# Performance work log

Measured on AMD Instinct MI355X. Metric: run time of the kernel, lower is better.

## Reference

```python
import jax, jax.numpy as jnp
import numpy as np

D_MODEL = 768
NUM_HEADS = 12
D_K = D_MODEL // NUM_HEADS


def setup_inputs() -> dict:
    key = jax.random.key(0)
    ks = jax.random.split(key, 9)
    B, S = 2, 4096
    x = jax.random.normal(ks[0], (B, S, D_MODEL), dtype=jnp.float32)
    s = 1.0 / np.sqrt(D_MODEL)
    Wq = jax.random.normal(ks[1], (D_MODEL, D_MODEL), dtype=jnp.float32) * s
    Wk = jax.random.normal(ks[2], (D_MODEL, D_MODEL), dtype=jnp.float32) * s
    Wv = jax.random.normal(ks[3], (D_MODEL, D_MODEL), dtype=jnp.float32) * s
    Wo = jax.random.normal(ks[4], (D_MODEL, D_MODEL), dtype=jnp.float32) * s
    bq = jnp.zeros((D_MODEL,), dtype=jnp.float32)
    bk = jnp.zeros((D_MODEL,), dtype=jnp.float32)
    bv = jnp.zeros((D_MODEL,), dtype=jnp.float32)
    bo = jnp.zeros((D_MODEL,), dtype=jnp.float32)
    return {"x": x, "Wq": Wq, "bq": bq, "Wk": Wk, "bk": bk,
            "Wv": Wv, "bv": bv, "Wo": Wo, "bo": bo}


def _split_heads(t):
    B, S, _ = t.shape
    return t.reshape(B, S, NUM_HEADS, D_K).transpose(0, 2, 1, 3)  # [B,H,S,d_k]


def reference(x, Wq, bq, Wk, bk, Wv, bv, Wo, bo):
    Q = _split_heads(x @ Wq.T + bq)
    K = _split_heads(x @ Wk.T + bk)
    V = _split_heads(x @ Wv.T + bv)
    scale = 1.0 / jnp.sqrt(jnp.float32(D_K))
    scores = jnp.einsum('bhqd,bhkd->bhqk', Q, K) * scale  # [B,H,S,S]
    attn = jax.nn.softmax(scores, axis=-1)
    out = jnp.einsum('bhqk,bhkd->bhqd', attn, V)          # [B,H,S,d_k]
    B, _, S, _ = out.shape
    out = out.transpose(0, 2, 1, 3).reshape(B, S, D_MODEL)
    return out @ Wo.T + bo
```

## Files before the change

kernel.cpp:

```cpp
#include <hip/hip_runtime.h>
#include <hip/hip_bf16.h>
#include <stdint.h>

typedef __hip_bfloat16 bf16;
typedef __attribute__((ext_vector_type(8))) short short8;
typedef __attribute__((ext_vector_type(4))) float f32x4;
typedef __attribute__((ext_vector_type(16))) float f32x16;

#define MFMA16(a, b, c) __builtin_amdgcn_mfma_f32_16x16x32_bf16((a), (b), (c), 0, 0, 0)
#define MFMA32(a, b, c) __builtin_amdgcn_mfma_f32_32x32x16_bf16((a), (b), (c), 0, 0, 0)

__device__ __forceinline__ unsigned short f2bf(float f) {
  bf16 h = __float2bfloat16(f);
  unsigned short u;
  __builtin_memcpy(&u, &h, 2);
  return u;
}

__device__ __forceinline__ uint32_t cvtpk(float lo, float hi) {
  uint32_t r;
  asm("v_cvt_pk_bf16_f32 %0, %1, %2" : "=v"(r) : "v"(lo), "v"(hi));
  return r;
}

__device__ __forceinline__ void pl32swap(uint32_t& a, uint32_t& b) {
  asm volatile("v_permlane32_swap_b32 %0, %1" : "+v"(a), "+v"(b));
}

__device__ __forceinline__ void gload_lds16(const void* g, void* l) {
  __builtin_amdgcn_global_load_lds(
      (const __attribute__((address_space(1))) uint32_t*)g,
      (__attribute__((address_space(3))) uint32_t*)l, 16, 0, 0);
}

__device__ __forceinline__ int swz_chunk(int row, int c) { return c ^ (row & 7); }

__global__ __launch_bounds__(256) void cvt_all(
    const float* __restrict__ x,
    const float* __restrict__ w0, const float* __restrict__ w1,
    const float* __restrict__ w2, const float* __restrict__ w3,
    bf16* __restrict__ xo,
    bf16* __restrict__ o0, bf16* __restrict__ o1,
    bf16* __restrict__ o2, bf16* __restrict__ o3) {
  int idx = blockIdx.x * 256 + threadIdx.x;
  const float* src;
  bf16* dst;
  int i;
  if (idx < 1572864) {
    src = x; dst = xo; i = idx;
  } else {
    int r = idx - 1572864;
    int w = r / 147456;
    i = r - w * 147456;
    src = (w == 0) ? w0 : (w == 1) ? w1 : (w == 2) ? w2 : w3;
    dst = (w == 0) ? o0 : (w == 1) ? o1 : (w == 2) ? o2 : o3;
  }
  float4 v = ((const float4*)src)[i];
  ushort4 u;
  u.x = f2bf(v.x); u.y = f2bf(v.y); u.z = f2bf(v.z); u.w = f2bf(v.w);
  ((ushort4*)dst)[i] = u;
}

__global__ __launch_bounds__(256, 4) void gemm_qkv(
    const bf16* __restrict__ A,
    const bf16* __restrict__ Wqb, const bf16* __restrict__ Wkb,
    const bf16* __restrict__ Wvb,
    const float* __restrict__ bq, const float* __restrict__ bk,
    const float* __restrict__ bv,
    bf16* __restrict__ Qh, bf16* __restrict__ Kh, bf16* __restrict__ Vtt,
    float sq) {
  __shared__ bf16 As[128 * 64];
  __shared__ bf16 Bs[128 * 64];
  const int tid = threadIdx.x;
  const int lane = tid & 63, wid = tid >> 6;
  const int wr = wid >> 1, wc = wid & 1;
  const int l15 = lane & 15, lhi = lane >> 4;
  const int tm = blockIdx.x * 128;
  const int by = blockIdx.y;
  const int seg = by / 6;
  const int tn = (by - seg * 6) * 128;

  const bf16* B = (seg == 0) ? Wqb : (seg == 1) ? Wkb : Wvb;
  const float* bias = (seg == 0) ? bq : (seg == 1) ? bk : bv;
  const float scale = (seg == 0) ? sq : 1.0f;
  const int K = 768;

  f32x4 zero = {0.f, 0.f, 0.f, 0.f};
  f32x4 acc[4][4];
  for (int i = 0; i < 4; ++i)
    for (int j = 0; j < 4; ++j) acc[i][j] = zero;

  for (int k0 = 0; k0 < K; k0 += 64) {
    __syncthreads();
    for (int it = 0; it < 4; ++it) {
      int o = (tid + it * 256) << 4;
      int row = o >> 7, c = (o >> 4) & 7;
      int sw = swz_chunk(row, c) << 4;
      gload_lds16((const char*)A + (((size_t)(tm + row) * K + k0) << 1) + sw, (char*)As + o);
      gload_lds16((const char*)B + (((size_t)(tn + row) * K + k0) << 1) + sw, (char*)Bs + o);
    }
    __syncthreads();
    for (int ks = 0; ks < 2; ++ks) {
      short8 af[4], bfr[4];
      for (int mi = 0; mi < 4; ++mi) {
        int row = wr * 64 + mi * 16 + l15;
        af[mi] = *(const short8*)((const char*)As + row * 128 +
                                  (swz_chunk(row, ks * 4 + lhi) << 4));
      }
      for (int ni = 0; ni < 4; ++ni) {
        int row = wc * 64 + ni * 16 + l15;
        bfr[ni] = *(const short8*)((const char*)Bs + row * 128 +
                                   (swz_chunk(row, ks * 4 + lhi) << 4));
      }
      for (int mi = 0; mi < 4; ++mi)
        for (int ni = 0; ni < 4; ++ni)
          acc[mi][ni] = MFMA16(af[mi], bfr[ni], acc[mi][ni]);
    }
  }

  if (seg == 2) {
    for (int mi = 0; mi < 4; ++mi)
      for (int ni = 0; ni < 4; ++ni) {
        int m0 = tm + wr * 64 + mi * 16 + lhi * 4;
        int n = tn + wc * 64 + ni * 16 + l15;
        int b = m0 >> 12, s = m0 & 4095, hh = n >> 6, d = n & 63;
        float bia = bias[n];
        ushort4 us;
        us.x = f2bf(acc[mi][ni][0] + bia);
        us.y = f2bf(acc[mi][ni][1] + bia);
        us.z = f2bf(acc[mi][ni][2] + bia);
        us.w = f2bf(acc[mi][ni][3] + bia);
        size_t e = (size_t)(b * 12 + hh) * 262144 + (size_t)(s >> 6) * 4096 +
                   (size_t)((s >> 3) & 7) * 512 + d * 8 + (s & 7);
        *(ushort4*)(Vtt + e) = us;
      }
  } else {
    bf16* dst = (seg == 0) ? Qh : Kh;
    for (int mi = 0; mi < 4; ++mi)
      for (int ni = 0; ni < 4; ++ni)
        for (int j = 0; j < 4; ++j) {
          int m = tm + wr * 64 + mi * 16 + lhi * 4 + j;
          int n = tn + wc * 64 + ni * 16 + l15;
          float v = (acc[mi][ni][j] + bias[n]) * scale;
          int b = m >> 12, s = m & 4095, hh = n >> 6, d = n & 63;
          dst[(((size_t)(b * 12 + hh) * 4096 + s) << 6) + d] = __float2bfloat16(v);
        }
  }
}

__global__ __launch_bounds__(256, 4) void gemm_wo(
    const bf16* __restrict__ A, const bf16* __restrict__ B,
    const float* __restrict__ bias, float* __restrict__ C) {
  __shared__ bf16 As[128 * 64];
  __shared__ bf16 Bs[64 * 64];
  const int tid = threadIdx.x;
  const int lane = tid & 63, wid = tid >> 6;
  const int l15 = lane & 15, lhi = lane >> 4;
  const int tm = blockIdx.x * 128, tn = blockIdx.y * 64;
  const int K = 768;

  f32x4 zero = {0.f, 0.f, 0.f, 0.f};
  f32x4 acc[2][4];
  for (int i = 0; i < 2; ++i)
    for (int j = 0; j < 4; ++j) acc[i][j] = zero;

  for (int k0 = 0; k0 < K; k0 += 64) {
    __syncthreads();
    for (int it = 0; it < 4; ++it) {
      int o = (tid + it * 256) << 4;
      int row = o >> 7, c = (o >> 4) & 7;
      int sw = swz_chunk(row, c) << 4;
      gload_lds16((const char*)A + (((size_t)(tm + row) * K + k0) << 1) + sw, (char*)As + o);
    }
    for (int it = 0; it < 2; ++it) {
      int o = (tid + it * 256) << 4;
      int row = o >> 7, c = (o >> 4) & 7;
      int sw = swz_chunk(row, c) << 4;
      gload_lds16((const char*)B + (((size_t)(tn + row) * K + k0) << 1) + sw, (char*)Bs + o);
    }
    __syncthreads();
    for (int ks = 0; ks < 2; ++ks) {
      short8 af[2], bfr[4];
      for (int mi = 0; mi < 2; ++mi) {
        int row = wid * 32 + mi * 16 + l15;
        af[mi] = *(const short8*)((const char*)As + row * 128 +
                                  (swz_chunk(row, ks * 4 + lhi) << 4));
      }
      for (int ni = 0; ni < 4; ++ni) {
        int row = ni * 16 + l15;
        bfr[ni] = *(const short8*)((const char*)Bs + row * 128 +
                                   (swz_chunk(row, ks * 4 + lhi) << 4));
      }
      for (int mi = 0; mi < 2; ++mi)
        for (int ni = 0; ni < 4; ++ni)
          acc[mi][ni] = MFMA16(af[mi], bfr[ni], acc[mi][ni]);
    }
  }

  for (int mi = 0; mi < 2; ++mi)
    for (int ni = 0; ni < 4; ++ni)
      for (int j = 0; j < 4; ++j) {
        int m = tm + wid * 32 + mi * 16 + lhi * 4 + j;
        int n = tn + ni * 16 + l15;
        C[(size_t)m * 768 + n] = acc[mi][ni][j] + bias[n];
      }
}

__global__ __launch_bounds__(256, 3) void attn_kernel(
    const bf16* __restrict__ Qh, const bf16* __restrict__ Kh,
    const bf16* __restrict__ VTT, bf16* __restrict__ AO) {
  __shared__ float4 smem4[34816 / 16];
  char* smraw = (char*)smem4;
#define KT(b) (smraw + (b) * 8192)
#define VT(b) (smraw + 16384 + (b) * 8192)
  float* OX = (float*)smraw;

  const int tid = threadIdx.x;
  const int lane = tid & 63, wid = tid >> 6;
  const int l31 = lane & 31, h = lane >> 5;
  const int qsub = wid & 1, kvh = wid >> 1;

  const int i = blockIdx.x;
  const int xcd = i & 7, slot = i >> 3;
  const int bh = xcd * 3 + (slot >> 5);
  const int qt = slot & 31;

  const size_t hb = (size_t)bh * 262144;
  const bf16* Qb = Qh + hb;
  const bf16* Kb = Kh + hb;
  const char* Vbc = (const char*)(VTT + hb);
  const int qb = qt * 128 + qsub * 64;

  short8 qf[2][4];
#pragma unroll
  for (int j = 0; j < 2; ++j)
#pragma unroll
    for (int ki = 0; ki < 4; ++ki)
      qf[j][ki] = *(const short8*)((const char*)Qb + (size_t)(qb + 32 * j + l31) * 128 +
                                   ki * 32 + h * 16);

  f32x16 z16;
  for (int i2 = 0; i2 < 16; ++i2) z16[i2] = 0.f;
  f32x16 o00 = z16, o01 = z16, o10 = z16, o11 = z16;
  float psum0 = 0.f, psum1 = 0.f;

  const int krow = kvh * 32 + l31;

  for (int it = 0; it < 2; ++it) {
    int o = (tid + it * 256) << 4;
    int row = o >> 7, c = (o >> 4) & 7;
    gload_lds16((const char*)Kb + row * 128 + (swz_chunk(row, c) << 4), KT(0) + o);
    gload_lds16(Vbc + (swz_chunk(row, c) << 10) + (row << 4), VT(0) + o);
  }
  __syncthreads();

  int cur = 0;
  for (int kt = 0; kt < 64; ++kt) {
    if (kt < 63) {
      const char* Kg = (const char*)(Kb + (size_t)(kt + 1) * 4096);
      const char* Vg = Vbc + (size_t)(kt + 1) * 8192;
      char* Kd = KT(cur ^ 1);
      char* Vd = VT(cur ^ 1);
      for (int it = 0; it < 2; ++it) {
        int o = (tid + it * 256) << 4;
        int row = o >> 7, c = (o >> 4) & 7;
        gload_lds16(Kg + row * 128 + (swz_chunk(row, c) << 4), Kd + o);
        gload_lds16(Vg + (swz_chunk(row, c) << 10) + (row << 4), Vd + o);
      }
    }

    const char* Kl = KT(cur);
    const char* Vl = VT(cur);

    f32x16 s0, s1;
    __builtin_amdgcn_s_setprio(1);
    {
      short8 kf = *(const short8*)(Kl + krow * 128 + (swz_chunk(krow, h) << 4));
      s0 = MFMA32(kf, qf[0][0], z16);
      s1 = MFMA32(kf, qf[1][0], z16);
    }
#pragma unroll
    for (int ki = 1; ki < 4; ++ki) {
      short8 kf = *(const short8*)(Kl + krow * 128 + (swz_chunk(krow, 2 * ki + h) << 4));
      s0 = MFMA32(kf, qf[0][ki], s0);
      s1 = MFMA32(kf, qf[1][ki], s1);
    }
    __builtin_amdgcn_s_setprio(0);

    short8 pb[2][2];
#pragma unroll
    for (int j = 0; j < 2; ++j) {
#pragma unroll
      for (int kk = 0; kk < 2; ++kk) {
        float p[8];
#pragma unroll
        for (int e = 0; e < 8; ++e)
          p[e] = __builtin_amdgcn_exp2f(j ? s1[8 * kk + e] : s0[8 * kk + e]);
        float ps = ((p[0] + p[1]) + (p[2] + p[3])) + ((p[4] + p[5]) + (p[6] + p[7]));
        if (j) psum1 += ps; else psum0 += ps;
        uint32_t A0 = cvtpk(p[0], p[1]), A1 = cvtpk(p[2], p[3]);
        uint32_t B0 = cvtpk(p[4], p[5]), B1 = cvtpk(p[6], p[7]);
        pl32swap(A0, B0);
        pl32swap(A1, B1);
        uint32_t w[4] = {A0, A1, B0, B1};
        short8 frag;
        __builtin_memcpy(&frag, w, 16);
        pb[j][kk] = frag;
      }
    }

    __builtin_amdgcn_s_setprio(1);
#pragma unroll
    for (int kk = 0; kk < 2; ++kk) {
      short8 v0 = *(const short8*)(Vl + l31 * 128 +
                                   (swz_chunk(l31, 4 * kvh + 2 * kk + h) << 4));
      short8 v1 = *(const short8*)(Vl + (32 + l31) * 128 +
                                   (swz_chunk(32 + l31, 4 * kvh + 2 * kk + h) << 4));
      o00 = MFMA32(v0, pb[0][kk], o00);
      o01 = MFMA32(v0, pb[1][kk], o01);
      o10 = MFMA32(v1, pb[0][kk], o10);
      o11 = MFMA32(v1, pb[1][kk], o11);
    }
    __builtin_amdgcn_s_setprio(0);

    __syncthreads();
    cur ^= 1;
  }

  psum0 += __shfl_xor(psum0, 32);
  psum1 += __shfl_xor(psum1, 32);

  float* W = OX + (size_t)(qsub * 64 + lane) * 68;
  if (kvh == 1) {
#pragma unroll
    for (int g = 0; g < 4; ++g) {
      *(float4*)(W + 0 * 16 + 4 * g) = make_float4(o00[4*g], o00[4*g+1], o00[4*g+2], o00[4*g+3]);
      *(float4*)(W + 1 * 16 + 4 * g) = make_float4(o01[4*g], o01[4*g+1], o01[4*g+2], o01[4*g+3]);
      *(float4*)(W + 2 * 16 + 4 * g) = make_float4(o10[4*g], o10[4*g+1], o10[4*g+2], o10[4*g+3]);
      *(float4*)(W + 3 * 16 + 4 * g) = make_float4(o11[4*g], o11[4*g+1], o11[4*g+2], o11[4*g+3]);
    }
    W[64] = psum0;
    W[65] = psum1;
  }
  __syncthreads();
  if (kvh == 0) {
#pragma unroll
    for (int g = 0; g < 4; ++g) {
      float4 a0 = *(const float4*)(W + 0 * 16 + 4 * g);
      float4 a1 = *(const float4*)(W + 1 * 16 + 4 * g);
      float4 a2 = *(const float4*)(W + 2 * 16 + 4 * g);
      float4 a3 = *(const float4*)(W + 3 * 16 + 4 * g);
      o00[4*g] += a0.x; o00[4*g+1] += a0.y; o00[4*g+2] += a0.z; o00[4*g+3] += a0.w;
      o01[4*g] += a1.x; o01[4*g+1] += a1.y; o01[4*g+2] += a1.z; o01[4*g+3] += a1.w;
      o10[4*g] += a2.x; o10[4*g+1] += a2.y; o10[4*g+2] += a2.z; o10[4*g+3] += a2.w;
      o11[4*g] += a3.x; o11[4*g+1] += a3.y; o11[4*g+2] += a3.z; o11[4*g+3] += a3.w;
    }
    psum0 += W[64];
    psum1 += W[65];
    float pinv0 = 1.0f / psum0;
    float pinv1 = 1.0f / psum1;

    const int b = bh / 12, hd = bh % 12;
#pragma unroll
    for (int j = 0; j < 2; ++j) {
      int q = qb + 32 * j + l31;
      char* base = (char*)AO + (((size_t)(b * 4096 + q)) * 768 + hd * 64) * 2;
      float pv = j ? pinv1 : pinv0;
#pragma unroll
      for (int t = 0; t < 2; ++t) {
#pragma unroll
        for (int u = 0; u < 4; ++u) {
          ushort4 us;
          float v0 = (t ? (j ? o11[4*u+0] : o10[4*u+0]) : (j ? o01[4*u+0] : o00[4*u+0]));
          float v1 = (t ? (j ? o11[4*u+1] : o10[4*u+1]) : (j ? o01[4*u+1] : o00[4*u+1]));
          float v2 = (t ? (j ? o11[4*u+2] : o10[4*u+2]) : (j ? o01[4*u+2] : o00[4*u+2]));
          float v3 = (t ? (j ? o11[4*u+3] : o10[4*u+3]) : (j ? o01[4*u+3] : o00[4*u+3]));
          us.x = f2bf(v0 * pv);
          us.y = f2bf(v1 * pv);
          us.z = f2bf(v2 * pv);
          us.w = f2bf(v3 * pv);
          int d0 = 32 * t + 8 * u + 4 * h;
          *(ushort4*)(base + d0 * 2) = us;
        }
      }
    }
  }
#undef KT
#undef VT
}

extern "C" void kernel_launch(void* const* d_in, const int* in_sizes, int n_in,
                              void* d_out, int out_size, void* d_ws, size_t ws_size,
                              hipStream_t stream) {
  (void)in_sizes; (void)n_in; (void)out_size; (void)ws_size;
  const float* x  = (const float*)d_in[0];
  const float* Wq = (const float*)d_in[1];
  const float* bq = (const float*)d_in[2];
  const float* Wk = (const float*)d_in[3];
  const float* bk = (const float*)d_in[4];
  const float* Wv = (const float*)d_in[5];
  const float* bv = (const float*)d_in[6];
  const float* Wo = (const float*)d_in[7];
  const float* bo = (const float*)d_in[8];

  char* ws = (char*)d_ws;
  bf16* Qh  = (bf16*)(ws + 0);
  bf16* Kh  = (bf16*)(ws + 12582912);
  bf16* VTT = (bf16*)(ws + 25165824);
  bf16* xb  = (bf16*)(ws + 37748736);
  bf16* Wqb = (bf16*)(ws + 50331648);
  bf16* Wkb = (bf16*)(ws + 51511296);
  bf16* Wvb = (bf16*)(ws + 52690944);
  bf16* Wob = (bf16*)(ws + 53870592);
  bf16* AO  = xb;

  cvt_all<<<8448, 256, 0, stream>>>(x, Wq, Wk, Wv, Wo, xb, Wqb, Wkb, Wvb, Wob);

  const float SQ = 0.125f * 1.4426950408889634f;
  dim3 gq(64, 18);
  gemm_qkv<<<gq, 256, 0, stream>>>(xb, Wqb, Wkb, Wvb, bq, bk, bv,
                                   Qh, Kh, VTT, SQ);
  attn_kernel<<<768, 256, 0, stream>>>(Qh, Kh, VTT, AO);
  dim3 gw(64, 12);
  gemm_wo<<<gw, 256, 0, stream>>>(AO, Wob, bo, (float*)d_out);
}
```

Baseline: 180.3 us.

## Software-pipeline attention loop so QK of next tile overlaps PV of previous

```diff
diff --git a/kernel.cpp b/kernel.cpp
--- a/kernel.cpp
+++ b/kernel.cpp
@@ -209,10 +209,10 @@
 __global__ __launch_bounds__(256, 3) void attn_kernel(
     const bf16* __restrict__ Qh, const bf16* __restrict__ Kh,
     const bf16* __restrict__ VTT, bf16* __restrict__ AO) {
-  __shared__ float4 smem4[34816 / 16];
+  __shared__ float4 smem4[40960 / 16];
   char* smraw = (char*)smem4;
-#define KT(b) (smraw + (b) * 8192)
-#define VT(b) (smraw + 16384 + (b) * 8192)
+#define KTB(b) (smraw + (b) * 8192)
+#define VTB(b) (smraw + 16384 + (b) * 8192)
   float* OX = (float*)smraw;
 
   const int tid = threadIdx.x;
@@ -246,86 +246,120 @@
 
   const int krow = kvh * 32 + l31;
 
-  for (int it = 0; it < 2; ++it) {
-    int o = (tid + it * 256) << 4;
-    int row = o >> 7, c = (o >> 4) & 7;
-    gload_lds16((const char*)Kb + row * 128 + (swz_chunk(row, c) << 4), KT(0) + o);
-    gload_lds16(Vbc + (swz_chunk(row, c) << 10) + (row << 4), VT(0) + o);
-  }
+#define STAGE_K(kt, dstb)                                                  \
+  for (int it = 0; it < 2; ++it) {                                         \
+    int o = (tid + it * 256) << 4;                                         \
+    int row = o >> 7, c = (o >> 4) & 7;                                    \
+    gload_lds16((const char*)Kb + (size_t)(kt) * 4096 * 2 / 2 * 2 + 0 +    \
+                    (size_t)(kt) * 0 + (size_t)(kt) * 8192 - (size_t)(kt) * 8192 + \
+                    (size_t)(kt) * 8192 + row * 128 + (swz_chunk(row, c) << 4), \
+                (dstb) + o);                                               \
+  }
+#undef STAGE_K
+#define STAGE_K(kt, dstb)                                                  \
+  for (int it = 0; it < 2; ++it) {                                         \
+    int o = (tid + it * 256) << 4;                                         \
+    int row = o >> 7, c = (o >> 4) & 7;                                    \
+    gload_lds16((const char*)Kb + (size_t)(kt) * 8192 + row * 128 +        \
+                    (swz_chunk(row, c) << 4),                              \
+                (dstb) + o);                                               \
+  }
+#define STAGE_V(kt, dstb)                                                  \
+  for (int it = 0; it < 2; ++it) {                                         \
+    int o = (tid + it * 256) << 4;                                         \
+    int row = o >> 7, c = (o >> 4) & 7;                                    \
+    gload_lds16(Vbc + (size_t)(kt) * 8192 + (swz_chunk(row, c) << 10) +    \
+                    (row << 4),                                            \
+                (dstb) + o);                                               \
+  }
+
+#define DO_QK(Kl)                                                          \
+  {                                                                        \
+    short8 kf = *(const short8*)((Kl) + krow * 128 + (swz_chunk(krow, h) << 4)); \
+    s0 = MFMA32(kf, qf[0][0], z16);                                        \
+    s1 = MFMA32(kf, qf[1][0], z16);                                        \
+  }                                                                        \
+  _Pragma("unroll")                                                        \
+  for (int ki = 1; ki < 4; ++ki) {                                         \
+    short8 kf = *(const short8*)((Kl) + krow * 128 +                       \
+                                 (swz_chunk(krow, 2 * ki + h) << 4));      \
+    s0 = MFMA32(kf, qf[0][ki], s0);                                        \
+    s1 = MFMA32(kf, qf[1][ki], s1);                                        \
+  }
+
+#define DO_PV(Vl)                                                          \
+  _Pragma("unroll")                                                        \
+  for (int kk = 0; kk < 2; ++kk) {                                         \
+    short8 v0 = *(const short8*)((Vl) + l31 * 128 +                        \
+                                 (swz_chunk(l31, 4 * kvh + 2 * kk + h) << 4)); \
+    short8 v1 = *(const short8*)((Vl) + (32 + l31) * 128 +                 \
+                                 (swz_chunk(32 + l31, 4 * kvh + 2 * kk + h) << 4)); \
+    o00 = MFMA32(v0, pb[0][kk], o00);                                      \
+    o01 = MFMA32(v0, pb[1][kk], o01);                                      \
+    o10 = MFMA32(v1, pb[0][kk], o10);                                      \
+    o11 = MFMA32(v1, pb[1][kk], o11);                                      \
+  }
+
+#define DO_EXP()                                                           \
+  _Pragma("unroll")                                                        \
+  for (int j = 0; j < 2; ++j) {                                            \
+    _Pragma("unroll")                                                      \
+    for (int kk = 0; kk < 2; ++kk) {                                       \
+      float p[8];                                                          \
+      _Pragma("unroll")                                                    \
+      for (int e = 0; e < 8; ++e)                                          \
+        p[e] = __builtin_amdgcn_exp2f(j ? s1[8 * kk + e] : s0[8 * kk + e]); \
+      float ps = ((p[0] + p[1]) + (p[2] + p[3])) + ((p[4] + p[5]) + (p[6] + p[7])); \
+      if (j) psum1 += ps; else psum0 += ps;                                \
+      uint32_t A0 = cvtpk(p[0], p[1]), A1 = cvtpk(p[2], p[3]);             \
+      uint32_t B0 = cvtpk(p[4], p[5]), B1 = cvtpk(p[6], p[7]);             \
+      pl32swap(A0, B0);                                                    \
+      pl32swap(A1, B1);                                                    \
+      uint32_t w_[4] = {A0, A1, B0, B1};                                   \
+      short8 frag;                                                         \
+      __builtin_memcpy(&frag, w_, 16);                                     \
+      pb[j][kk] = frag;                                                    \
+    }                                                                      \
+  }
+
+  short8 pb[2][2];
+
+  STAGE_K(0, KTB(0));
+  STAGE_V(0, VTB(0));
   __syncthreads();
-
-  int cur = 0;
-  for (int kt = 0; kt < 64; ++kt) {
-    if (kt < 63) {
-      const char* Kg = (const char*)(Kb + (size_t)(kt + 1) * 4096);
-      const char* Vg = Vbc + (size_t)(kt + 1) * 8192;
-      char* Kd = KT(cur ^ 1);
-      char* Vd = VT(cur ^ 1);
-      for (int it = 0; it < 2; ++it) {
-        int o = (tid + it * 256) << 4;
-        int row = o >> 7, c = (o >> 4) & 7;
-        gload_lds16(Kg + row * 128 + (swz_chunk(row, c) << 4), Kd + o);
-        gload_lds16(Vg + (swz_chunk(row, c) << 10) + (row << 4), Vd + o);
-      }
-    }
-
-    const char* Kl = KT(cur);
-    const char* Vl = VT(cur);
-
+  STAGE_K(1, KTB(1));
+  STAGE_V(1, VTB(1));
+  {
     f32x16 s0, s1;
     __builtin_amdgcn_s_setprio(1);
-    {
-      short8 kf = *(const short8*)(Kl + krow * 128 + (swz_chunk(krow, h) << 4));
-      s0 = MFMA32(kf, qf[0][0], z16);
-      s1 = MFMA32(kf, qf[1][0], z16);
-    }
-#pragma unroll
-    for (int ki = 1; ki < 4; ++ki) {
-      short8 kf = *(const short8*)(Kl + krow * 128 + (swz_chunk(krow, 2 * ki + h) << 4));
-      s0 = MFMA32(kf, qf[0][ki], s0);
-      s1 = MFMA32(kf, qf[1][ki], s1);
-    }
+    DO_QK(KTB(0));
     __builtin_amdgcn_s_setprio(0);
-
-    short8 pb[2][2];
-#pragma unroll
-    for (int j = 0; j < 2; ++j) {
-#pragma unroll
-      for (int kk = 0; kk < 2; ++kk) {
-        float p[8];
-#pragma unroll
-        for (int e = 0; e < 8; ++e)
-          p[e] = __builtin_amdgcn_exp2f(j ? s1[8 * kk + e] : s0[8 * kk + e]);
-        float ps = ((p[0] + p[1]) + (p[2] + p[3])) + ((p[4] + p[5]) + (p[6] + p[7]));
-        if (j) psum1 += ps; else psum0 += ps;
-        uint32_t A0 = cvtpk(p[0], p[1]), A1 = cvtpk(p[2], p[3]);
-        uint32_t B0 = cvtpk(p[4], p[5]), B1 = cvtpk(p[6], p[7]);
-        pl32swap(A0, B0);
-        pl32swap(A1, B1);
-        uint32_t w[4] = {A0, A1, B0, B1};
-        short8 frag;
-        __builtin_memcpy(&frag, w, 16);
-        pb[j][kk] = frag;
-      }
-    }
-
+    DO_EXP();
+  }
+
+  char* Vp = VTB(0);
+  char* Vc = VTB(1);
+  char* Vn = VTB(2);
+  for (int kt = 1; kt < 64; ++kt) {
+    __syncthreads();
+    if (kt < 63) {
+      STAGE_K(kt + 1, KTB((kt + 1) & 1));
+      STAGE_V(kt + 1, Vn);
+    }
+    f32x16 s0, s1;
     __builtin_amdgcn_s_setprio(1);
-#pragma unroll
-    for (int kk = 0; kk < 2; ++kk) {
-      short8 v0 = *(const short8*)(Vl + l31 * 128 +
-                                   (swz_chunk(l31, 4 * kvh + 2 * kk + h) << 4));
-      short8 v1 = *(const short8*)(Vl + (32 + l31) * 128 +
-                                   (swz_chunk(32 + l31, 4 * kvh + 2 * kk + h) << 4));
-      o00 = MFMA32(v0, pb[0][kk], o00);
-      o01 = MFMA32(v0, pb[1][kk], o01);
-      o10 = MFMA32(v1, pb[0][kk], o10);
-      o11 = MFMA32(v1, pb[1][kk], o11);
-    }
+    DO_QK(KTB(kt & 1));
+    DO_PV(Vp);
     __builtin_amdgcn_s_setprio(0);
-
-    __syncthreads();
-    cur ^= 1;
-  }
+    DO_EXP();
+    char* t = Vp; Vp = Vc; Vc = Vn; Vn = t;
+  }
+  {
+    __builtin_amdgcn_s_setprio(1);
+    DO_PV(Vp);
+    __builtin_amdgcn_s_setprio(0);
+  }
+  __syncthreads();
 
   psum0 += __shfl_xor(psum0, 32);
   psum1 += __shfl_xor(psum1, 32);
@@ -385,8 +419,13 @@
       }
     }
   }
-#undef KT
-#undef VT
+#undef KTB
+#undef VTB
+#undef STAGE_K
+#undef STAGE_V
+#undef DO_QK
+#undef DO_PV
+#undef DO_EXP
 }
 
 extern "C" void kernel_launch(void* const* d_in, const int* in_sizes, int n_in,
```

After: 314.4 us. 74.3% more time.

## Split attention KV range in two and merge partials with combine kernel

Applied to the files above, without the earlier changes.

```diff
diff --git a/kernel.cpp b/kernel.cpp
--- a/kernel.cpp
+++ b/kernel.cpp
@@ -15,6 +15,13 @@
   unsigned short u;
   __builtin_memcpy(&u, &h, 2);
   return u;
+}
+
+__device__ __forceinline__ float bf2f(unsigned short u) {
+  uint32_t x = ((uint32_t)u) << 16;
+  float f;
+  __builtin_memcpy(&f, &x, 4);
+  return f;
 }
 
 __device__ __forceinline__ uint32_t cvtpk(float lo, float hi) {
@@ -206,9 +213,12 @@
       }
 }
 
+template <int SPLIT>
 __global__ __launch_bounds__(256, 3) void attn_kernel(
     const bf16* __restrict__ Qh, const bf16* __restrict__ Kh,
-    const bf16* __restrict__ VTT, bf16* __restrict__ AO) {
+    const bf16* __restrict__ VTT, bf16* __restrict__ AO,
+    bf16* __restrict__ OP0, bf16* __restrict__ OP1,
+    float* __restrict__ PS0, float* __restrict__ PS1) {
   __shared__ float4 smem4[34816 / 16];
   char* smraw = (char*)smem4;
 #define KT(b) (smraw + (b) * 8192)
@@ -222,8 +232,19 @@
 
   const int i = blockIdx.x;
   const int xcd = i & 7, slot = i >> 3;
-  const int bh = xcd * 3 + (slot >> 5);
-  const int qt = slot & 31;
+  int bh, qt, kvp;
+  if (SPLIT) {
+    bh = xcd * 3 + (slot >> 6);
+    int r = slot & 63;
+    qt = r >> 1;
+    kvp = r & 1;
+  } else {
+    bh = xcd * 3 + (slot >> 5);
+    qt = slot & 31;
+    kvp = 0;
+  }
+  const int NT = SPLIT ? 32 : 64;
+  const int kv0 = kvp * 32;
 
   const size_t hb = (size_t)bh * 262144;
   const bf16* Qb = Qh + hb;
@@ -249,16 +270,19 @@
   for (int it = 0; it < 2; ++it) {
     int o = (tid + it * 256) << 4;
     int row = o >> 7, c = (o >> 4) & 7;
-    gload_lds16((const char*)Kb + row * 128 + (swz_chunk(row, c) << 4), KT(0) + o);
-    gload_lds16(Vbc + (swz_chunk(row, c) << 10) + (row << 4), VT(0) + o);
+    gload_lds16((const char*)Kb + (size_t)kv0 * 8192 + row * 128 +
+                    (swz_chunk(row, c) << 4), KT(0) + o);
+    gload_lds16(Vbc + (size_t)kv0 * 8192 + (swz_chunk(row, c) << 10) + (row << 4),
+                VT(0) + o);
   }
   __syncthreads();
 
   int cur = 0;
-  for (int kt = 0; kt < 64; ++kt) {
-    if (kt < 63) {
-      const char* Kg = (const char*)(Kb + (size_t)(kt + 1) * 4096);
-      const char* Vg = Vbc + (size_t)(kt + 1) * 8192;
+  for (int kt = 0; kt < NT; ++kt) {
+    if (kt < NT - 1) {
+      const size_t akt = (size_t)(kv0 + kt + 1);
+      const char* Kg = (const char*)Kb + akt * 8192;
+      const char* Vg = Vbc + akt * 8192;
       char* Kd = KT(cur ^ 1);
       char* Vd = VT(cur ^ 1);
       for (int it = 0; it < 2; ++it) {
@@ -357,42 +381,94 @@
     }
     psum0 += W[64];
     psum1 += W[65];
-    float pinv0 = 1.0f / psum0;
-    float pinv1 = 1.0f / psum1;
 
     const int b = bh / 12, hd = bh % 12;
-#pragma unroll
-    for (int j = 0; j < 2; ++j) {
-      int q = qb + 32 * j + l31;
-      char* base = (char*)AO + (((size_t)(b * 4096 + q)) * 768 + hd * 64) * 2;
-      float pv = j ? pinv1 : pinv0;
-#pragma unroll
-      for (int t = 0; t < 2; ++t) {
-#pragma unroll
-        for (int u = 0; u < 4; ++u) {
-          ushort4 us;
-          float v0 = (t ? (j ? o11[4*u+0] : o10[4*u+0]) : (j ? o01[4*u+0] : o00[4*u+0]));
-          float v1 = (t ? (j ? o11[4*u+1] : o10[4*u+1]) : (j ? o01[4*u+1] : o00[4*u+1]));
-          float v2 = (t ? (j ? o11[4*u+2] : o10[4*u+2]) : (j ? o01[4*u+2] : o00[4*u+2]));
-          float v3 = (t ? (j ? o11[4*u+3] : o10[4*u+3]) : (j ? o01[4*u+3] : o00[4*u+3]));
-          us.x = f2bf(v0 * pv);
-          us.y = f2bf(v1 * pv);
-          us.z = f2bf(v2 * pv);
-          us.w = f2bf(v3 * pv);
-          int d0 = 32 * t + 8 * u + 4 * h;
-          *(ushort4*)(base + d0 * 2) = us;
+    if (SPLIT) {
+      bf16* OPp = kvp ? OP1 : OP0;
+      float* PSp = kvp ? PS1 : PS0;
+#pragma unroll
+      for (int j = 0; j < 2; ++j) {
+        int q = qb + 32 * j + l31;
+        char* base = (char*)OPp + (((size_t)(b * 4096 + q)) * 768 + hd * 64) * 2;
+#pragma unroll
+        for (int t = 0; t < 2; ++t) {
+#pragma unroll
+          for (int u = 0; u < 4; ++u) {
+            ushort4 us;
+            float v0 = (t ? (j ? o11[4*u+0] : o10[4*u+0]) : (j ? o01[4*u+0] : o00[4*u+0]));
+            float v1 = (t ? (j ? o11[4*u+1] : o10[4*u+1]) : (j ? o01[4*u+1] : o00[4*u+1]));
+            float v2 = (t ? (j ? o11[4*u+2] : o10[4*u+2]) : (j ? o01[4*u+2] : o00[4*u+2]));
+            float v3 = (t ? (j ? o11[4*u+3] : o10[4*u+3]) : (j ? o01[4*u+3] : o00[4*u+3]));
+            us.x = f2bf(v0); us.y = f2bf(v1); us.z = f2bf(v2); us.w = f2bf(v3);
+            int d0 = 32 * t + 8 * u + 4 * h;
+            *(ushort4*)(base + d0 * 2) = us;
+          }
+        }
+        PSp[(size_t)bh * 4096 + q] = j ? psum1 : psum0;
+      }
+    } else {
+      float pinv0 = 1.0f / psum0;
+      float pinv1 = 1.0f / psum1;
+#pragma unroll
+      for (int j = 0; j < 2; ++j) {
+        int q = qb + 32 * j + l31;
+        char* base = (char*)AO + (((size_t)(b * 4096 + q)) * 768 + hd * 64) * 2;
+        float pv = j ? pinv1 : pinv0;
+#pragma unroll
+        for (int t = 0; t < 2; ++t) {
+#pragma unroll
+          for (int u = 0; u < 4; ++u) {
+            ushort4 us;
+            float v0 = (t ? (j ? o11[4*u+0] : o10[4*u+0]) : (j ? o01[4*u+0] : o00[4*u+0]));
+            float v1 = (t ? (j ? o11[4*u+1] : o10[4*u+1]) : (j ? o01[4*u+1] : o00[4*u+1]));
+            float v2 = (t ? (j ? o11[4*u+2] : o10[4*u+2]) : (j ? o01[4*u+2] : o00[4*u+2]));
+            float v3 = (t ? (j ? o11[4*u+3] : o10[4*u+3]) : (j ? o01[4*u+3] : o00[4*u+3]));
+            us.x = f2bf(v0 * pv); us.y = f2bf(v1 * pv);
+            us.z = f2bf(v2 * pv); us.w = f2bf(v3 * pv);
+            int d0 = 32 * t + 8 * u + 4 * h;
+            *(ushort4*)(base + d0 * 2) = us;
+          }
         }
       }
     }
   }
 #undef KT
 #undef VT
+}
+
+__global__ __launch_bounds__(256) void combine_kernel(
+    const bf16* __restrict__ OP0, const bf16* __restrict__ OP1,
+    const float* __restrict__ PS0, const float* __restrict__ PS1,
+    bf16* __restrict__ AO) {
+  int t = blockIdx.x * 256 + threadIdx.x;
+  size_t e0 = (size_t)t * 8;
+  int row = (int)(e0 / 768);
+  int col = (int)(e0 - (size_t)row * 768);
+  int hd = col >> 6;
+  int bh = (row >> 12) * 12 + hd;
+  int q = row & 4095;
+  float r = 1.0f / (PS0[(size_t)bh * 4096 + q] + PS1[(size_t)bh * 4096 + q]);
+  ushort4 a0 = *(const ushort4*)(OP0 + e0);
+  ushort4 a1 = *(const ushort4*)(OP0 + e0 + 4);
+  ushort4 b0 = *(const ushort4*)(OP1 + e0);
+  ushort4 b1 = *(const ushort4*)(OP1 + e0 + 4);
+  ushort4 o0, o1;
+  o0.x = f2bf((bf2f(a0.x) + bf2f(b0.x)) * r);
+  o0.y = f2bf((bf2f(a0.y) + bf2f(b0.y)) * r);
+  o0.z = f2bf((bf2f(a0.z) + bf2f(b0.z)) * r);
+  o0.w = f2bf((bf2f(a0.w) + bf2f(b0.w)) * r);
+  o1.x = f2bf((bf2f(a1.x) + bf2f(b1.x)) * r);
+  o1.y = f2bf((bf2f(a1.y) + bf2f(b1.y)) * r);
+  o1.z = f2bf((bf2f(a1.z) + bf2f(b1.z)) * r);
+  o1.w = f2bf((bf2f(a1.w) + bf2f(b1.w)) * r);
+  *(ushort4*)(AO + e0) = o0;
+  *(ushort4*)(AO + e0 + 4) = o1;
 }
 
 extern "C" void kernel_launch(void* const* d_in, const int* in_sizes, int n_in,
                               void* d_out, int out_size, void* d_ws, size_t ws_size,
                               hipStream_t stream) {
-  (void)in_sizes; (void)n_in; (void)out_size; (void)ws_size;
+  (void)in_sizes; (void)n_in; (void)out_size;
   const float* x  = (const float*)d_in[0];
   const float* Wq = (const float*)d_in[1];
   const float* bq = (const float*)d_in[2];
@@ -412,7 +488,11 @@
   bf16* Wkb = (bf16*)(ws + 51511296);
   bf16* Wvb = (bf16*)(ws + 52690944);
   bf16* Wob = (bf16*)(ws + 53870592);
-  bf16* AO  = xb;
+  bf16* OP0 = xb;
+  bf16* OP1 = (bf16*)(ws + 55050240);
+  float* PS0 = (float*)(ws + 67633152);
+  float* PS1 = (float*)(ws + 68026368);
+  const size_t NEED = 68419584;
 
   cvt_all<<<8448, 256, 0, stream>>>(x, Wq, Wk, Wv, Wo, xb, Wqb, Wkb, Wvb, Wob);
 
@@ -420,7 +500,17 @@
   dim3 gq(64, 18);
   gemm_qkv<<<gq, 256, 0, stream>>>(xb, Wqb, Wkb, Wvb, bq, bk, bv,
                                    Qh, Kh, VTT, SQ);
-  attn_kernel<<<768, 256, 0, stream>>>(Qh, Kh, VTT, AO);
   dim3 gw(64, 12);
-  gemm_wo<<<gw, 256, 0, stream>>>(AO, Wob, bo, (float*)d_out);
-}
+  if (ws_size >= NEED) {
+    attn_kernel<1><<<1536, 256, 0, stream>>>(Qh, Kh, VTT, nullptr,
+                                             OP0, OP1, PS0, PS1);
+    bf16* AOq = Qh;
+    combine_kernel<<<3072, 256, 0, stream>>>(OP0, OP1, PS0, PS1, AOq);
+    gemm_wo<<<gw, 256, 0, stream>>>(AOq, Wob, bo, (float*)d_out);
+  } else {
+    bf16* AO = xb;
+    attn_kernel<0><<<768, 256, 0, stream>>>(Qh, Kh, VTT, AO,
+                                            nullptr, nullptr, nullptr, nullptr);
+    gemm_wo<<<gw, 256, 0, stream>>>(AO, Wob, bo, (float*)d_out);
+  }
+}
```

Result: slower. 188.3 us (+4.4%).
